# Kernel optimization log

Hardware: AMD Instinct MI355X
Metric: run time of the kernel (lower is better)

## Reference

```python
import jax, jax.numpy as jnp
import numpy as np

NUM_HEADS = 8
EPS = 1e-6


def hamilton(a, b):
    # Quaternion (Hamilton) product on the last axis (size 4), broadcasting leading dims.
    aw, ax, ay, az = a[..., 0], a[..., 1], a[..., 2], a[..., 3]
    bw, bx, by, bz = b[..., 0], b[..., 1], b[..., 2], b[..., 3]
    return jnp.stack([
        aw * bw - ax * bx - ay * by - az * bz,
        aw * bx + ax * bw + ay * bz - az * by,
        aw * by - ax * bz + ay * bw + az * bx,
        aw * bz + ax * by - ay * bx + az * bw,
    ], axis=-1)


def setup_inputs() -> dict:
    key = jax.random.key(0)
    ks = jax.random.split(key, 7)
    B, L, E = 2, 384, 512
    s = 1.0 / np.sqrt(E)
    return {
        'x': jax.random.normal(ks[0], (B, L, E), dtype=jnp.float32),
        'Wq': jax.random.normal(ks[1], (E, E), dtype=jnp.float32) * s,
        'Wk': jax.random.normal(ks[2], (E, E), dtype=jnp.float32) * s,
        'Wv': jax.random.normal(ks[3], (E, E), dtype=jnp.float32) * s,
        'Wo': jax.random.normal(ks[4], (E, E), dtype=jnp.float32) * s,
        'dde_w': jax.random.normal(ks[5], (4, 4), dtype=jnp.float32) * 0.5,
        'dde_b': jnp.zeros((4,), dtype=jnp.float32),
    }


def reference(x, Wq, Wk, Wv, Wo, dde_w, dde_b):
    B, L, E = x.shape
    H = NUM_HEADS
    hd = E // H            # head_dim
    c = hd // 4            # quaternion atoms per head

    def proj_quat(W):
        # x @ W^T  -> split heads -> quaternion atoms: (B*H, L, c, 4)
        y = jnp.einsum('ble,fe->blf', x, W)
        y = y.reshape(B, L, H, hd).transpose(0, 2, 1, 3)  # (B,H,L,hd)
        return y.reshape(B * H, L, c, 4)

    q = proj_quat(Wq)
    k = proj_quat(Wk)
    v = proj_quat(Wv)

    # Broadcasted Hamilton product: (BH, L, L, c, 4)
    interference = hamilton(q[:, :, None, :, :], k[:, None, :, :, :])
    norm = jnp.linalg.norm(interference, axis=-1, keepdims=True) + EPS
    spinor = interference / norm

    # Discrete decision gate: mean over atoms -> (BH, L, L, 4) -> sigmoid(linear)
    gate_in = spinor.mean(axis=-2)
    gate = jax.nn.sigmoid(jnp.einsum('blmq,pq->blmp', gate_in, dde_w) + dde_b)
    spinor = spinor * gate[:, :, :, None, :]

    # Value aggregation: Hamilton product with v, summed over key positions j
    ctx = hamilton(spinor, v[:, None, :, :, :]).sum(axis=2)  # (BH, L, c, 4)

    ctx = ctx.reshape(B, H, L, hd).transpose(0, 2, 1, 3).reshape(B, L, E)
    return jnp.einsum('ble,fe->blf', ctx, Wo)
```

## Files before the change

kernel.cpp:

```cpp
#include <hip/hip_runtime.h>
#include <math.h>

#define L_SEQ 384
#define E_DIM 512
#define NHEAD 8
#define NBH   16
#define HD    64
#define LOG2E 1.44269504f

typedef __attribute__((ext_vector_type(8))) __bf16 bf16x8;
typedef __attribute__((ext_vector_type(8))) _Float16 f16x8;
typedef __attribute__((ext_vector_type(4))) float f32x4;

union u4h8 { uint4 u; f16x8 h; };

__device__ __forceinline__ float uniform_f(float v) {
  return __uint_as_float(__builtin_amdgcn_readfirstlane(__float_as_uint(v)));
}

__device__ __forceinline__ unsigned f2bf(float f) {
  unsigned u = __float_as_uint(f);
  return (u + 0x7FFFu + ((u >> 16) & 1u)) >> 16;
}

__device__ __forceinline__ unsigned ror16(unsigned x) { return (x >> 16) | (x << 16); }

__device__ __forceinline__ float dpp_xor1(float x) {
  return __int_as_float(__builtin_amdgcn_mov_dpp(__float_as_int(x), 0xB1, 0xF, 0xF, 0));
}
__device__ __forceinline__ float dpp_xor2(float x) {
  return __int_as_float(__builtin_amdgcn_mov_dpp(__float_as_int(x), 0x4E, 0xF, 0xF, 0));
}
template <int IMM>
__device__ __forceinline__ float swz_xor(float x) {
  return __int_as_float(__builtin_amdgcn_ds_swizzle(__float_as_int(x), IMM));
}

__device__ __forceinline__ size_t pidx(int row, int k, int Kd) {
  return ((((size_t)(row >> 4) * (Kd >> 5) + (k >> 5)) * 4 + ((k >> 3) & 3)) * 16
          + (row & 15)) * 8 + (k & 7);
}

__global__ __launch_bounds__(256) void to_bf16_all(
    const float* __restrict__ x, const float* __restrict__ Wq,
    const float* __restrict__ Wk, const float* __restrict__ Wv,
    const float* __restrict__ Wo, unsigned short* __restrict__ dst1,
    unsigned short* __restrict__ dst2, float* __restrict__ outz)
{
  int e0 = (blockIdx.x * 256 + threadIdx.x) * 4;
  if (e0 >= 1835008) return;
  if (e0 >= 1441792) {
    *(float4*)(outz + (e0 - 1441792)) = make_float4(0.f, 0.f, 0.f, 0.f);
    return;
  }
  const float* src; unsigned short* d; int s;
  if (e0 < 393216)       { src = x;  s = e0;           d = dst1; }
  else if (e0 < 655360)  { src = Wq; s = e0 - 393216;  d = dst1 + 393216; }
  else if (e0 < 917504)  { src = Wk; s = e0 - 655360;  d = dst1 + 655360; }
  else if (e0 < 1179648) { src = Wv; s = e0 - 917504;  d = dst1 + 917504; }
  else                   { src = Wo; s = e0 - 1179648; d = dst2; }
  float4 v = *(const float4*)(src + s);
  unsigned lo = f2bf(v.x) | (f2bf(v.y) << 16);
  unsigned hi = f2bf(v.z) | (f2bf(v.w) << 16);
  int row = s >> 9, k = s & 511;
  *(uint2*)(d + pidx(row, k, 512)) = make_uint2(lo, hi);
}

template <int NTN, int MODE>
__global__ __launch_bounds__(256) void gemm_mfma(
    const __bf16* __restrict__ A, const __bf16* __restrict__ B0,
    const __bf16* __restrict__ B1, const __bf16* __restrict__ B2,
    float* __restrict__ C0, float* __restrict__ C1, float* __restrict__ C2,
    int M, int N, int K)
{
  const int z = blockIdx.z;
  const __bf16* Bm = (MODE == 2) ? B0 : (z == 0) ? B0 : (z == 1) ? B1 : B2;
  float* Cp = (MODE == 2) ? C0 : (z == 0) ? C0 : (z == 1) ? C1 : C2;

  const int tid = threadIdx.x;
  const int wave = tid >> 6, lane = tid & 63;
  const int m0 = blockIdx.y * 64 + wave * 16;
  const int n0 = blockIdx.x * (16 * NTN);
  const int mr = lane & 15, quad = lane >> 4;
  const int KT = K >> 5;
  const int kb0 = (MODE == 2) ? z * 4 : 0;
  const int KL = (MODE == 2) ? 4 : KT;

  f32x4 acc[NTN];
  #pragma unroll
  for (int nt = 0; nt < NTN; ++nt) acc[nt] = (f32x4){0.f, 0.f, 0.f, 0.f};

  const __bf16* ap = A + ((size_t)(m0 >> 4) * KT + kb0) * 512 + lane * 8;
  const __bf16* bp = Bm + ((size_t)(n0 >> 4) * KT + kb0) * 512 + lane * 8;

  #pragma unroll 4
  for (int ks = 0; ks < KL; ++ks) {
    bf16x8 a = *(const bf16x8*)(ap + (size_t)ks * 512);
    #pragma unroll
    for (int nt = 0; nt < NTN; ++nt) {
      bf16x8 b = *(const bf16x8*)(bp + ((size_t)nt * KT + ks) * 512);
      acc[nt] = __builtin_amdgcn_mfma_f32_16x16x32_bf16(a, b, acc[nt], 0, 0, 0);
    }
  }

  if (MODE == 2) {
    #pragma unroll
    for (int nt = 0; nt < NTN; ++nt) {
      int n = n0 + nt * 16 + mr;
      #pragma unroll
      for (int r = 0; r < 4; ++r) {
        int m = m0 + quad * 4 + r;
        __hip_atomic_fetch_add(&Cp[(size_t)m * N + n], acc[nt][r],
                               __ATOMIC_RELAXED, __HIP_MEMORY_SCOPE_AGENT);
      }
    }
  } else {
    _Float16* Hp = (_Float16*)Cp;
    #pragma unroll
    for (int nt = 0; nt < NTN; ++nt) {
      int n = n0 + nt * 16 + mr;
      #pragma unroll
      for (int r = 0; r < 4; ++r) {
        float val = acc[nt][r];
        float s = val * val;
        s += dpp_xor1(s);
        s += dpp_xor2(s);
        float sc = (z == 2) ? 1.f : __builtin_amdgcn_rsqf(fmaxf(s, 1e-30f));
        int m = m0 + quad * 4 + r;
        int b = m / L_SEQ, l = m - b * L_SEQ;
        int row = (b * NHEAD + (n >> 6)) * L_SEQ + l;
        Hp[pidx(row, n & 63, 64)] = (_Float16)(val * sc);
      }
    }
  }
}

__global__ __launch_bounds__(256) void z_build(
    const _Float16* __restrict__ khh, const _Float16* __restrict__ vhh,
    _Float16* __restrict__ Z0)
{
  const int tid = threadIdx.x;
  const int l = blockIdx.x * 64 + (tid & 63);
  const int a = blockIdx.y * 4 + (tid >> 6);
  const int bh = blockIdx.z;

  size_t off = pidx(bh * L_SEQ + l, a * 4, 64);
  union { uint2 u; _Float16 h[4]; } kk, vv;
  kk.u = *(const uint2*)(khh + off);
  vv.u = *(const uint2*)(vhh + off);

  float kb[4] = {(float)kk.h[0], (float)kk.h[1], (float)kk.h[2], (float)kk.h[3]};
  float ve[4] = {(float)vv.h[0], (float)vv.h[1], (float)vv.h[2], (float)vv.h[3]};
  _Float16* zp = Z0 + (size_t)bh * (256 * 384);
  #pragma unroll
  for (int b = 0; b < 4; ++b)
    #pragma unroll
    for (int e = 0; e < 4; ++e)
      zp[pidx(a * 16 + b * 4 + e, l, 384)] = (_Float16)(kb[b] * ve[e]);
}

__global__ __launch_bounds__(256) void gate_pv(
    const _Float16* __restrict__ qhh, const _Float16* __restrict__ khh,
    const _Float16* __restrict__ Z0, const float* __restrict__ dde_w,
    const float* __restrict__ dde_b, unsigned short* __restrict__ CTXB)
{
  __shared__ _Float16 gbuf[2][4096];
  __shared__ float qs[16][65];

  const int tid = threadIdx.x, w = tid >> 6, lane = tid & 63;
  const int mr = lane & 15, quad = lane >> 4;
  const int bh = blockIdx.y, ib = blockIdx.x;
  const int i0 = ib * 16;

  {
    int il = tid >> 4, k4 = (tid & 15) * 4;
    union { uint2 u; _Float16 h[4]; } cv;
    cv.u = *(const uint2*)(qhh + pidx(bh * L_SEQ + i0 + il, k4, 64));
    qs[il][k4 + 0] = (float)cv.h[0]; qs[il][k4 + 1] = (float)cv.h[1];
    qs[il][k4 + 2] = (float)cv.h[2]; qs[il][k4 + 3] = (float)cv.h[3];
  }

  float wn[16], bn[4];
  #pragma unroll
  for (int t = 0; t < 16; ++t) wn[t] = uniform_f(dde_w[t]) * (-LOG2E * 0.0625f);
  #pragma unroll
  for (int c = 0; c < 4; ++c) bn[c] = uniform_f(dde_b[c]) * (-LOG2E);

  u4h8 fr[4][2];
  {
    const _Float16* ap = qhh + ((size_t)(bh * 24 + ib)) * 2 * 512 + lane * 8;
    #pragma unroll
    for (int ks = 0; ks < 2; ++ks) {
      uint4 qa = *(const uint4*)(ap + ks * 512);
      unsigned s0 = ror16(qa.x), s1 = ror16(qa.y), s2 = ror16(qa.z), s3 = ror16(qa.w);
      fr[0][ks].u = make_uint4(qa.x ^ 0x80000000u, qa.y ^ 0x80008000u,
                               qa.z ^ 0x80000000u, qa.w ^ 0x80008000u);
      fr[1][ks].u = make_uint4(s0, s1 ^ 0x00008000u, s2, s3 ^ 0x00008000u);
      fr[2][ks].u = make_uint4(qa.y, qa.x ^ 0x80000000u, qa.w, qa.z ^ 0x80000000u);
      fr[3][ks].u = make_uint4(s1 ^ 0x80000000u, s0, s3 ^ 0x80000000u, s2);
    }
  }

  const int bq = mr >> 2, e = mr & 3;
  unsigned msk[4];
  #pragma unroll
  for (int c = 0; c < 4; ++c)
    msk[c] = ((((0x284Eu >> (c * 4 + bq)) ^ (0xC6A0u >> (c * 4 + e))) & 1u) << 31);

  f32x4 acc[4][4];
  #pragma unroll
  for (int c = 0; c < 4; ++c)
    #pragma unroll
    for (int nt = 0; nt < 4; ++nt) acc[c][nt] = (f32x4){0.f, 0.f, 0.f, 0.f};

  const int jl = w * 16 + mr;
  const int gw = (jl >> 3) * 128 + (jl & 7) + quad * 32;

  #pragma unroll 2
  for (int ch = 0; ch < 6; ++ch) {
    u4h8 zb[2][4];
    #pragma unroll
    for (int ks2 = 0; ks2 < 2; ++ks2)
      #pragma unroll
      for (int nt = 0; nt < 4; ++nt)
        zb[ks2][nt].h = *(const f16x8*)(Z0 + (size_t)bh * (256 * 384)
                         + (((size_t)(w * 4 + nt) * 12 + ch * 2 + ks2) * 512) + lane * 8);

    const _Float16* bp = khh + ((size_t)(bh * 24 + ch * 4 + w)) * 2 * 512 + lane * 8;
    u4h8 kb[2];
    kb[0].h = *(const f16x8*)(bp);
    kb[1].h = *(const f16x8*)(bp + 512);
    f32x4 accS[4];
    #pragma unroll
    for (int c = 0; c < 4; ++c) {
      accS[c] = (f32x4){0.f, 0.f, 0.f, 0.f};
      accS[c] = __builtin_amdgcn_mfma_f32_16x16x32_f16(fr[c][0].h, kb[0].h, accS[c], 0, 0, 0);
      accS[c] = __builtin_amdgcn_mfma_f32_16x16x32_f16(fr[c][1].h, kb[1].h, accS[c], 0, 0, 0);
    }

    #pragma unroll
    for (int r = 0; r < 4; ++r) {
      float S0 = accS[0][r], S1 = accS[1][r], S2 = accS[2][r], S3 = accS[3][r];
      #pragma unroll
      for (int c = 0; c < 4; ++c) {
        float n = bn[c] + wn[c*4+0]*S0 + wn[c*4+1]*S1 + wn[c*4+2]*S2 + wn[c*4+3]*S3;
        float g = __builtin_amdgcn_rcpf(1.f + __builtin_amdgcn_exp2f(n));
        gbuf[ch & 1][c * 1024 + gw + r * 8] = (_Float16)g;
      }
    }
    __syncthreads();

    #pragma unroll
    for (int ks2 = 0; ks2 < 2; ++ks2) {
      #pragma unroll
      for (int c = 0; c < 4; ++c) {
        f16x8 aa = *(const f16x8*)&gbuf[ch & 1][c * 1024 + ks2 * 512 + lane * 8];
        #pragma unroll
        for (int nt = 0; nt < 4; ++nt)
          acc[c][nt] = __builtin_amdgcn_mfma_f32_16x16x32_f16(aa, zb[ks2][nt].h, acc[c][nt], 0, 0, 0);
      }
    }
  }

  const int bb_ = bh >> 3, hh = bh & 7;
  #pragma unroll
  for (int nt = 0; nt < 4; ++nt) {
    #pragma unroll
    for (int r = 0; r < 4; ++r) {
      int il = quad * 4 + r;
      float pb[4];
      #pragma unroll
      for (int c = 0; c < 4; ++c) {
        float sq = __uint_as_float(
            __float_as_uint(qs[il][w * 16 + nt * 4 + (bq ^ c)]) ^ msk[c]);
        float v = sq * acc[c][nt][r];
        v += swz_xor<0x101F>(v);
        v += swz_xor<0x201F>(v);
        pb[c] = v;
      }
      float q0 = pb[0] + dpp_xor1(pb[1]);
      float q1 = pb[1] + dpp_xor1(pb[0]);
      float q2 = pb[2] + dpp_xor1(pb[3]);
      float q3 = pb[3] + dpp_xor1(pb[2]);
      float r0 = q0 + dpp_xor2(q2);
      float r1 = q1 + dpp_xor2(q3);
      float r2 = q2 + dpp_xor2(q0);
      float r3 = q3 + dpp_xor2(q1);
      if (mr == 0) {
        unsigned lo = f2bf(r0) | (f2bf(r1) << 16);
        unsigned hi = f2bf(r2) | (f2bf(r3) << 16);
        *(uint2*)&CTXB[pidx(bb_ * L_SEQ + i0 + il,
                            hh * HD + w * 16 + nt * 4, 512)] = make_uint2(lo, hi);
      }
    }
  }
}

extern "C" void kernel_launch(void* const* d_in, const int* in_sizes, int n_in,
                              void* d_out, int out_size, void* d_ws, size_t ws_size,
                              hipStream_t stream)
{
  const float* x     = (const float*)d_in[0];
  const float* Wq    = (const float*)d_in[1];
  const float* Wk    = (const float*)d_in[2];
  const float* Wv    = (const float*)d_in[3];
  const float* Wo    = (const float*)d_in[4];
  const float* dde_w = (const float*)d_in[5];
  const float* dde_b = (const float*)d_in[6];
  float* out = (float*)d_out;

  char* ws = (char*)d_ws;
  unsigned short* Wob  = (unsigned short*)(ws + 0);
  _Float16* qhh = (_Float16*)(ws + 524288);
  _Float16* khh = (_Float16*)(ws + 1310720);
  _Float16* Z0h = (_Float16*)(ws + 2097152);
  _Float16* vhh = (_Float16*)(ws + 5242880);
  unsigned short* CTXB = (unsigned short*)(ws + 5242880);
  unsigned short* xb  = (unsigned short*)(ws + 6029312);
  unsigned short* Wqb = (unsigned short*)(ws + 6815744);
  unsigned short* Wkb = (unsigned short*)(ws + 7340032);
  unsigned short* Wvb = (unsigned short*)(ws + 7864320);

  to_bf16_all<<<1792, 256, 0, stream>>>(x, Wq, Wk, Wv, Wo, xb, Wob, out);

  gemm_mfma<1, 1><<<dim3(32, 12, 3), 256, 0, stream>>>(
      (const __bf16*)xb, (const __bf16*)Wqb, (const __bf16*)Wkb, (const __bf16*)Wvb,
      (float*)qhh, (float*)khh, (float*)vhh, 2 * L_SEQ, E_DIM, E_DIM);

  z_build<<<dim3(6, 4, 16), 256, 0, stream>>>(khh, vhh, Z0h);

  gate_pv<<<dim3(24, 16), 256, 0, stream>>>(qhh, khh, Z0h, dde_w, dde_b, CTXB);

  gemm_mfma<2, 2><<<dim3(16, 12, 4), 256, 0, stream>>>(
      (const __bf16*)CTXB, (const __bf16*)Wob, nullptr, nullptr,
      out, nullptr, nullptr, 2 * L_SEQ, E_DIM, E_DIM);
}
```

Baseline: 102.8 us.

## Split gate_pv over key halves and reduce partials inside output GEMM

The gate/value kernel now splits the key-position loop into two halves across a new grid dimension, doubling block count to fill more compute units. Each half writes fp32 partial context to its own slab, and a dedicated output GEMM sums the two slabs and converts to bf16 while loading its A operand. This trades extra global memory traffic for the partial slabs for higher parallelism in the main attention-like kernel. The QKV GEMM is also specialised into a non-templated kernel without behaviour change.

```diff
diff --git a/kernel.cpp b/kernel.cpp
--- a/kernel.cpp
+++ b/kernel.cpp
@@ -66,72 +66,48 @@
   *(uint2*)(d + pidx(row, k, 512)) = make_uint2(lo, hi);
 }
 
-template <int NTN, int MODE>
-__global__ __launch_bounds__(256) void gemm_mfma(
+__global__ __launch_bounds__(256) void gemm_qkv(
     const __bf16* __restrict__ A, const __bf16* __restrict__ B0,
     const __bf16* __restrict__ B1, const __bf16* __restrict__ B2,
     float* __restrict__ C0, float* __restrict__ C1, float* __restrict__ C2,
     int M, int N, int K)
 {
   const int z = blockIdx.z;
-  const __bf16* Bm = (MODE == 2) ? B0 : (z == 0) ? B0 : (z == 1) ? B1 : B2;
-  float* Cp = (MODE == 2) ? C0 : (z == 0) ? C0 : (z == 1) ? C1 : C2;
+  const __bf16* Bm = (z == 0) ? B0 : (z == 1) ? B1 : B2;
+  float* Cp = (z == 0) ? C0 : (z == 1) ? C1 : C2;
 
   const int tid = threadIdx.x;
   const int wave = tid >> 6, lane = tid & 63;
   const int m0 = blockIdx.y * 64 + wave * 16;
-  const int n0 = blockIdx.x * (16 * NTN);
+  const int n0 = blockIdx.x * 16;
   const int mr = lane & 15, quad = lane >> 4;
   const int KT = K >> 5;
-  const int kb0 = (MODE == 2) ? z * 4 : 0;
-  const int KL = (MODE == 2) ? 4 : KT;
-
-  f32x4 acc[NTN];
-  #pragma unroll
-  for (int nt = 0; nt < NTN; ++nt) acc[nt] = (f32x4){0.f, 0.f, 0.f, 0.f};
-
-  const __bf16* ap = A + ((size_t)(m0 >> 4) * KT + kb0) * 512 + lane * 8;
-  const __bf16* bp = Bm + ((size_t)(n0 >> 4) * KT + kb0) * 512 + lane * 8;
+
+  f32x4 acc = (f32x4){0.f, 0.f, 0.f, 0.f};
+
+  const __bf16* ap = A + (size_t)(m0 >> 4) * KT * 512 + lane * 8;
+  const __bf16* bp = Bm + (size_t)(n0 >> 4) * KT * 512 + lane * 8;
 
   #pragma unroll 4
-  for (int ks = 0; ks < KL; ++ks) {
+  for (int ks = 0; ks < KT; ++ks) {
     bf16x8 a = *(const bf16x8*)(ap + (size_t)ks * 512);
-    #pragma unroll
-    for (int nt = 0; nt < NTN; ++nt) {
-      bf16x8 b = *(const bf16x8*)(bp + ((size_t)nt * KT + ks) * 512);
-      acc[nt] = __builtin_amdgcn_mfma_f32_16x16x32_bf16(a, b, acc[nt], 0, 0, 0);
-    }
-  }
-
-  if (MODE == 2) {
-    #pragma unroll
-    for (int nt = 0; nt < NTN; ++nt) {
-      int n = n0 + nt * 16 + mr;
-      #pragma unroll
-      for (int r = 0; r < 4; ++r) {
-        int m = m0 + quad * 4 + r;
-        __hip_atomic_fetch_add(&Cp[(size_t)m * N + n], acc[nt][r],
-                               __ATOMIC_RELAXED, __HIP_MEMORY_SCOPE_AGENT);
-      }
-    }
-  } else {
-    _Float16* Hp = (_Float16*)Cp;
-    #pragma unroll
-    for (int nt = 0; nt < NTN; ++nt) {
-      int n = n0 + nt * 16 + mr;
-      #pragma unroll
-      for (int r = 0; r < 4; ++r) {
-        float val = acc[nt][r];
-        float s = val * val;
-        s += dpp_xor1(s);
-        s += dpp_xor2(s);
-        float sc = (z == 2) ? 1.f : __builtin_amdgcn_rsqf(fmaxf(s, 1e-30f));
-        int m = m0 + quad * 4 + r;
-        int b = m / L_SEQ, l = m - b * L_SEQ;
-        int row = (b * NHEAD + (n >> 6)) * L_SEQ + l;
-        Hp[pidx(row, n & 63, 64)] = (_Float16)(val * sc);
-      }
-    }
+    bf16x8 b = *(const bf16x8*)(bp + (size_t)ks * 512);
+    acc = __builtin_amdgcn_mfma_f32_16x16x32_bf16(a, b, acc, 0, 0, 0);
+  }
+
+  _Float16* Hp = (_Float16*)Cp;
+  int n = n0 + mr;
+  #pragma unroll
+  for (int r = 0; r < 4; ++r) {
+    float val = acc[r];
+    float s = val * val;
+    s += dpp_xor1(s);
+    s += dpp_xor2(s);
+    float sc = (z == 2) ? 1.f : __builtin_amdgcn_rsqf(fmaxf(s, 1e-30f));
+    int m = m0 + quad * 4 + r;
+    int b = m / L_SEQ, l = m - b * L_SEQ;
+    int row = (b * NHEAD + (n >> 6)) * L_SEQ + l;
+    Hp[pidx(row, n & 63, 64)] = (_Float16)(val * sc);
   }
 }
 
@@ -162,14 +138,14 @@
 __global__ __launch_bounds__(256) void gate_pv(
     const _Float16* __restrict__ qhh, const _Float16* __restrict__ khh,
     const _Float16* __restrict__ Z0, const float* __restrict__ dde_w,
-    const float* __restrict__ dde_b, unsigned short* __restrict__ CTXB)
+    const float* __restrict__ dde_b, float* __restrict__ CTXS)
 {
   __shared__ _Float16 gbuf[2][4096];
   __shared__ float qs[16][65];
 
   const int tid = threadIdx.x, w = tid >> 6, lane = tid & 63;
   const int mr = lane & 15, quad = lane >> 4;
-  const int bh = blockIdx.y, ib = blockIdx.x;
+  const int bh = blockIdx.y, ib = blockIdx.x, jh = blockIdx.z;
   const int i0 = ib * 16;
 
   {
@@ -216,8 +192,9 @@
   const int jl = w * 16 + mr;
   const int gw = (jl >> 3) * 128 + (jl & 7) + quad * 32;
 
-  #pragma unroll 2
-  for (int ch = 0; ch < 6; ++ch) {
+  #pragma unroll
+  for (int ci = 0; ci < 3; ++ci) {
+    const int ch = jh * 3 + ci;
     u4h8 zb[2][4];
     #pragma unroll
     for (int ks2 = 0; ks2 < 2; ++ks2)
@@ -245,7 +222,7 @@
       for (int c = 0; c < 4; ++c) {
         float n = bn[c] + wn[c*4+0]*S0 + wn[c*4+1]*S1 + wn[c*4+2]*S2 + wn[c*4+3]*S3;
         float g = __builtin_amdgcn_rcpf(1.f + __builtin_amdgcn_exp2f(n));
-        gbuf[ch & 1][c * 1024 + gw + r * 8] = (_Float16)g;
+        gbuf[ci & 1][c * 1024 + gw + r * 8] = (_Float16)g;
       }
     }
     __syncthreads();
@@ -254,7 +231,7 @@
     for (int ks2 = 0; ks2 < 2; ++ks2) {
       #pragma unroll
       for (int c = 0; c < 4; ++c) {
-        f16x8 aa = *(const f16x8*)&gbuf[ch & 1][c * 1024 + ks2 * 512 + lane * 8];
+        f16x8 aa = *(const f16x8*)&gbuf[ci & 1][c * 1024 + ks2 * 512 + lane * 8];
         #pragma unroll
         for (int nt = 0; nt < 4; ++nt)
           acc[c][nt] = __builtin_amdgcn_mfma_f32_16x16x32_f16(aa, zb[ks2][nt].h, acc[c][nt], 0, 0, 0);
@@ -263,6 +240,7 @@
   }
 
   const int bb_ = bh >> 3, hh = bh & 7;
+  float* slab = CTXS + (size_t)jh * 393216;
   #pragma unroll
   for (int nt = 0; nt < 4; ++nt) {
     #pragma unroll
@@ -287,11 +265,59 @@
       float r2 = q2 + dpp_xor2(q0);
       float r3 = q3 + dpp_xor2(q1);
       if (mr == 0) {
-        unsigned lo = f2bf(r0) | (f2bf(r1) << 16);
-        unsigned hi = f2bf(r2) | (f2bf(r3) << 16);
-        *(uint2*)&CTXB[pidx(bb_ * L_SEQ + i0 + il,
-                            hh * HD + w * 16 + nt * 4, 512)] = make_uint2(lo, hi);
+        *(float4*)&slab[pidx(bb_ * L_SEQ + i0 + il,
+                             hh * HD + w * 16 + nt * 4, 512)] =
+            make_float4(r0, r1, r2, r3);
       }
+    }
+  }
+}
+
+__global__ __launch_bounds__(256) void out_gemm(
+    const float* __restrict__ S0, const float* __restrict__ S1,
+    const __bf16* __restrict__ Wob, float* __restrict__ out)
+{
+  const int z = blockIdx.z;
+  const int tid = threadIdx.x;
+  const int wave = tid >> 6, lane = tid & 63;
+  const int m0 = blockIdx.y * 64 + wave * 16;
+  const int n0 = blockIdx.x * 32;
+  const int mr = lane & 15, quad = lane >> 4;
+  const int KT = 16;
+
+  f32x4 acc[2];
+  acc[0] = (f32x4){0.f, 0.f, 0.f, 0.f};
+  acc[1] = (f32x4){0.f, 0.f, 0.f, 0.f};
+
+  const size_t abase = ((size_t)(m0 >> 4) * KT + z * 4) * 512 + lane * 8;
+  const __bf16* bp = Wob + ((size_t)(n0 >> 4) * KT + z * 4) * 512 + lane * 8;
+
+  #pragma unroll
+  for (int ks = 0; ks < 4; ++ks) {
+    const float* a0 = S0 + abase + (size_t)ks * 512;
+    const float* a1 = S1 + abase + (size_t)ks * 512;
+    float4 x0 = *(const float4*)a0, x1 = *(const float4*)(a0 + 4);
+    float4 y0 = *(const float4*)a1, y1 = *(const float4*)(a1 + 4);
+    bf16x8 a;
+    a[0] = (__bf16)(x0.x + y0.x); a[1] = (__bf16)(x0.y + y0.y);
+    a[2] = (__bf16)(x0.z + y0.z); a[3] = (__bf16)(x0.w + y0.w);
+    a[4] = (__bf16)(x1.x + y1.x); a[5] = (__bf16)(x1.y + y1.y);
+    a[6] = (__bf16)(x1.z + y1.z); a[7] = (__bf16)(x1.w + y1.w);
+    #pragma unroll
+    for (int nt = 0; nt < 2; ++nt) {
+      bf16x8 b = *(const bf16x8*)(bp + ((size_t)nt * KT + ks) * 512);
+      acc[nt] = __builtin_amdgcn_mfma_f32_16x16x32_bf16(a, b, acc[nt], 0, 0, 0);
+    }
+  }
+
+  #pragma unroll
+  for (int nt = 0; nt < 2; ++nt) {
+    int n = n0 + nt * 16 + mr;
+    #pragma unroll
+    for (int r = 0; r < 4; ++r) {
+      int m = m0 + quad * 4 + r;
+      __hip_atomic_fetch_add(&out[(size_t)m * E_DIM + n], acc[nt][r],
+                             __ATOMIC_RELAXED, __HIP_MEMORY_SCOPE_AGENT);
     }
   }
 }
@@ -314,8 +340,8 @@
   _Float16* qhh = (_Float16*)(ws + 524288);
   _Float16* khh = (_Float16*)(ws + 1310720);
   _Float16* Z0h = (_Float16*)(ws + 2097152);
+  float* CTXS = (float*)(ws + 5242880);
   _Float16* vhh = (_Float16*)(ws + 5242880);
-  unsigned short* CTXB = (unsigned short*)(ws + 5242880);
   unsigned short* xb  = (unsigned short*)(ws + 6029312);
   unsigned short* Wqb = (unsigned short*)(ws + 6815744);
   unsigned short* Wkb = (unsigned short*)(ws + 7340032);
@@ -323,15 +349,14 @@
 
   to_bf16_all<<<1792, 256, 0, stream>>>(x, Wq, Wk, Wv, Wo, xb, Wob, out);
 
-  gemm_mfma<1, 1><<<dim3(32, 12, 3), 256, 0, stream>>>(
+  gemm_qkv<<<dim3(32, 12, 3), 256, 0, stream>>>(
       (const __bf16*)xb, (const __bf16*)Wqb, (const __bf16*)Wkb, (const __bf16*)Wvb,
       (float*)qhh, (float*)khh, (float*)vhh, 2 * L_SEQ, E_DIM, E_DIM);
 
   z_build<<<dim3(6, 4, 16), 256, 0, stream>>>(khh, vhh, Z0h);
 
-  gate_pv<<<dim3(24, 16), 256, 0, stream>>>(qhh, khh, Z0h, dde_w, dde_b, CTXB);
-
-  gemm_mfma<2, 2><<<dim3(16, 12, 4), 256, 0, stream>>>(
-      (const __bf16*)CTXB, (const __bf16*)Wob, nullptr, nullptr,
-      out, nullptr, nullptr, 2 * L_SEQ, E_DIM, E_DIM);
-}
+  gate_pv<<<dim3(24, 16, 2), 256, 0, stream>>>(qhh, khh, Z0h, dde_w, dde_b, CTXS);
+
+  out_gemm<<<dim3(16, 12, 4), 256, 0, stream>>>(
+      CTXS, CTXS + 393216, (const __bf16*)Wob, out);
+}
```

Measured after the change: 104.6 us. About the same (+1.7%).

## Fuse output projection into gate_pv epilogue with atomic accumulation

Applied to the files above, without the earlier changes.

The final Wo GEMM kernel is removed. Each gate_pv block now stages its 16x64 context tile in shared memory as bf16 and multiplies it by the head's slice of Wo with MFMA, atomically adding partial results into the zero-initialized output. This saves one kernel launch and the global round-trip of the context buffer. In exchange, every head contributes atomics to each output element (8-way contention), and gate_pv gets extra epilogue work and register pressure.

```diff
diff --git a/kernel.cpp b/kernel.cpp
--- a/kernel.cpp
+++ b/kernel.cpp
@@ -66,72 +66,48 @@
   *(uint2*)(d + pidx(row, k, 512)) = make_uint2(lo, hi);
 }
 
-template <int NTN, int MODE>
-__global__ __launch_bounds__(256) void gemm_mfma(
+__global__ __launch_bounds__(256) void gemm_qkv(
     const __bf16* __restrict__ A, const __bf16* __restrict__ B0,
     const __bf16* __restrict__ B1, const __bf16* __restrict__ B2,
     float* __restrict__ C0, float* __restrict__ C1, float* __restrict__ C2,
     int M, int N, int K)
 {
   const int z = blockIdx.z;
-  const __bf16* Bm = (MODE == 2) ? B0 : (z == 0) ? B0 : (z == 1) ? B1 : B2;
-  float* Cp = (MODE == 2) ? C0 : (z == 0) ? C0 : (z == 1) ? C1 : C2;
+  const __bf16* Bm = (z == 0) ? B0 : (z == 1) ? B1 : B2;
+  float* Cp = (z == 0) ? C0 : (z == 1) ? C1 : C2;
 
   const int tid = threadIdx.x;
   const int wave = tid >> 6, lane = tid & 63;
   const int m0 = blockIdx.y * 64 + wave * 16;
-  const int n0 = blockIdx.x * (16 * NTN);
+  const int n0 = blockIdx.x * 16;
   const int mr = lane & 15, quad = lane >> 4;
   const int KT = K >> 5;
-  const int kb0 = (MODE == 2) ? z * 4 : 0;
-  const int KL = (MODE == 2) ? 4 : KT;
-
-  f32x4 acc[NTN];
-  #pragma unroll
-  for (int nt = 0; nt < NTN; ++nt) acc[nt] = (f32x4){0.f, 0.f, 0.f, 0.f};
-
-  const __bf16* ap = A + ((size_t)(m0 >> 4) * KT + kb0) * 512 + lane * 8;
-  const __bf16* bp = Bm + ((size_t)(n0 >> 4) * KT + kb0) * 512 + lane * 8;
+
+  f32x4 acc = (f32x4){0.f, 0.f, 0.f, 0.f};
+
+  const __bf16* ap = A + (size_t)(m0 >> 4) * KT * 512 + lane * 8;
+  const __bf16* bp = Bm + (size_t)(n0 >> 4) * KT * 512 + lane * 8;
 
   #pragma unroll 4
-  for (int ks = 0; ks < KL; ++ks) {
+  for (int ks = 0; ks < KT; ++ks) {
     bf16x8 a = *(const bf16x8*)(ap + (size_t)ks * 512);
-    #pragma unroll
-    for (int nt = 0; nt < NTN; ++nt) {
-      bf16x8 b = *(const bf16x8*)(bp + ((size_t)nt * KT + ks) * 512);
-      acc[nt] = __builtin_amdgcn_mfma_f32_16x16x32_bf16(a, b, acc[nt], 0, 0, 0);
-    }
-  }
-
-  if (MODE == 2) {
-    #pragma unroll
-    for (int nt = 0; nt < NTN; ++nt) {
-      int n = n0 + nt * 16 + mr;
-      #pragma unroll
-      for (int r = 0; r < 4; ++r) {
-        int m = m0 + quad * 4 + r;
-        __hip_atomic_fetch_add(&Cp[(size_t)m * N + n], acc[nt][r],
-                               __ATOMIC_RELAXED, __HIP_MEMORY_SCOPE_AGENT);
-      }
-    }
-  } else {
-    _Float16* Hp = (_Float16*)Cp;
-    #pragma unroll
-    for (int nt = 0; nt < NTN; ++nt) {
-      int n = n0 + nt * 16 + mr;
-      #pragma unroll
-      for (int r = 0; r < 4; ++r) {
-        float val = acc[nt][r];
-        float s = val * val;
-        s += dpp_xor1(s);
-        s += dpp_xor2(s);
-        float sc = (z == 2) ? 1.f : __builtin_amdgcn_rsqf(fmaxf(s, 1e-30f));
-        int m = m0 + quad * 4 + r;
-        int b = m / L_SEQ, l = m - b * L_SEQ;
-        int row = (b * NHEAD + (n >> 6)) * L_SEQ + l;
-        Hp[pidx(row, n & 63, 64)] = (_Float16)(val * sc);
-      }
-    }
+    bf16x8 b = *(const bf16x8*)(bp + (size_t)ks * 512);
+    acc = __builtin_amdgcn_mfma_f32_16x16x32_bf16(a, b, acc, 0, 0, 0);
+  }
+
+  _Float16* Hp = (_Float16*)Cp;
+  int n = n0 + mr;
+  #pragma unroll
+  for (int r = 0; r < 4; ++r) {
+    float val = acc[r];
+    float s = val * val;
+    s += dpp_xor1(s);
+    s += dpp_xor2(s);
+    float sc = (z == 2) ? 1.f : __builtin_amdgcn_rsqf(fmaxf(s, 1e-30f));
+    int m = m0 + quad * 4 + r;
+    int b = m / L_SEQ, l = m - b * L_SEQ;
+    int row = (b * NHEAD + (n >> 6)) * L_SEQ + l;
+    Hp[pidx(row, n & 63, 64)] = (_Float16)(val * sc);
   }
 }
 
@@ -162,10 +138,12 @@
 __global__ __launch_bounds__(256) void gate_pv(
     const _Float16* __restrict__ qhh, const _Float16* __restrict__ khh,
     const _Float16* __restrict__ Z0, const float* __restrict__ dde_w,
-    const float* __restrict__ dde_b, unsigned short* __restrict__ CTXB)
+    const float* __restrict__ dde_b, const __bf16* __restrict__ Wob,
+    float* __restrict__ out)
 {
   __shared__ _Float16 gbuf[2][4096];
   __shared__ float qs[16][65];
+  __shared__ __bf16 ctx_lds[16][72];
 
   const int tid = threadIdx.x, w = tid >> 6, lane = tid & 63;
   const int mr = lane & 15, quad = lane >> 4;
@@ -262,7 +240,6 @@
     }
   }
 
-  const int bb_ = bh >> 3, hh = bh & 7;
   #pragma unroll
   for (int nt = 0; nt < 4; ++nt) {
     #pragma unroll
@@ -287,11 +264,36 @@
       float r2 = q2 + dpp_xor2(q0);
       float r3 = q3 + dpp_xor2(q1);
       if (mr == 0) {
-        unsigned lo = f2bf(r0) | (f2bf(r1) << 16);
-        unsigned hi = f2bf(r2) | (f2bf(r3) << 16);
-        *(uint2*)&CTXB[pidx(bb_ * L_SEQ + i0 + il,
-                            hh * HD + w * 16 + nt * 4, 512)] = make_uint2(lo, hi);
+        ctx_lds[il][w * 16 + nt * 4 + 0] = (__bf16)r0;
+        ctx_lds[il][w * 16 + nt * 4 + 1] = (__bf16)r1;
+        ctx_lds[il][w * 16 + nt * 4 + 2] = (__bf16)r2;
+        ctx_lds[il][w * 16 + nt * 4 + 3] = (__bf16)r3;
       }
+    }
+  }
+  __syncthreads();
+
+  const int bb_ = bh >> 3, hh = bh & 7;
+  const int m_base = bb_ * L_SEQ + i0;
+  bf16x8 af[2];
+  #pragma unroll
+  for (int ks2 = 0; ks2 < 2; ++ks2)
+    af[ks2] = *(const bf16x8*)&ctx_lds[mr][ks2 * 32 + quad * 8];
+  #pragma unroll
+  for (int nt2 = 0; nt2 < 8; ++nt2) {
+    const int ntile = w * 8 + nt2;
+    f32x4 accO = (f32x4){0.f, 0.f, 0.f, 0.f};
+    #pragma unroll
+    for (int ks2 = 0; ks2 < 2; ++ks2) {
+      bf16x8 b = *(const bf16x8*)(Wob + ((size_t)ntile * 16 + hh * 2 + ks2) * 512 + lane * 8);
+      accO = __builtin_amdgcn_mfma_f32_16x16x32_bf16(af[ks2], b, accO, 0, 0, 0);
+    }
+    const int n = ntile * 16 + mr;
+    #pragma unroll
+    for (int r = 0; r < 4; ++r) {
+      int m = m_base + quad * 4 + r;
+      __hip_atomic_fetch_add(&out[(size_t)m * E_DIM + n], accO[r],
+                             __ATOMIC_RELAXED, __HIP_MEMORY_SCOPE_AGENT);
     }
   }
 }
@@ -315,7 +317,6 @@
   _Float16* khh = (_Float16*)(ws + 1310720);
   _Float16* Z0h = (_Float16*)(ws + 2097152);
   _Float16* vhh = (_Float16*)(ws + 5242880);
-  unsigned short* CTXB = (unsigned short*)(ws + 5242880);
   unsigned short* xb  = (unsigned short*)(ws + 6029312);
   unsigned short* Wqb = (unsigned short*)(ws + 6815744);
   unsigned short* Wkb = (unsigned short*)(ws + 7340032);
@@ -323,15 +324,12 @@
 
   to_bf16_all<<<1792, 256, 0, stream>>>(x, Wq, Wk, Wv, Wo, xb, Wob, out);
 
-  gemm_mfma<1, 1><<<dim3(32, 12, 3), 256, 0, stream>>>(
+  gemm_qkv<<<dim3(32, 12, 3), 256, 0, stream>>>(
       (const __bf16*)xb, (const __bf16*)Wqb, (const __bf16*)Wkb, (const __bf16*)Wvb,
       (float*)qhh, (float*)khh, (float*)vhh, 2 * L_SEQ, E_DIM, E_DIM);
 
   z_build<<<dim3(6, 4, 16), 256, 0, stream>>>(khh, vhh, Z0h);
 
-  gate_pv<<<dim3(24, 16), 256, 0, stream>>>(qhh, khh, Z0h, dde_w, dde_b, CTXB);
-
-  gemm_mfma<2, 2><<<dim3(16, 12, 4), 256, 0, stream>>>(
-      (const __bf16*)CTXB, (const __bf16*)Wob, nullptr, nullptr,
-      out, nullptr, nullptr, 2 * L_SEQ, E_DIM, E_DIM);
-}
+  gate_pv<<<dim3(24, 16), 256, 0, stream>>>(
+      qhh, khh, Z0h, dde_w, dde_b, (const __bf16*)Wob, out);
+}
```

New measurement: 103.0 us. About the same (+0.2%).
